# Optimization experiments

Hardware: AMD Instinct MI355X
Metric: run time of the kernel (lower is better)

## Reference

```python
import jax, jax.numpy as jnp
import numpy as np

B, S, H = 64, 2048, 512
NEG_INF = -1e10


def setup_inputs() -> dict:
    key = jax.random.key(0)
    k1, k2, k3, k4, k5, k6 = jax.random.split(key, 6)
    return {
        "output": jax.random.normal(k1, (B, 1, H), dtype=jnp.float32),
        "encoder_outputs": jax.random.normal(k2, (B, S, H), dtype=jnp.float32),
        "encoder_sequence_lengths": jax.random.randint(k3, (B,), 1, S + 1, dtype=jnp.int32),
        "W1": jax.random.normal(k4, (H, H), dtype=jnp.float32) * (1.0 / np.sqrt(H)),
        "W2": jax.random.normal(k5, (H, H), dtype=jnp.float32) * (1.0 / np.sqrt(H)),
        "V": jax.random.normal(k6, (H, 1), dtype=jnp.float32) * (1.0 / np.sqrt(H)),
    }


def reference(output, encoder_outputs, encoder_sequence_lengths, W1, W2, V):
    # output: [B,1,H] decoder state (query); encoder_outputs: [B,S,H] (key & value)
    S_ = encoder_outputs.shape[1]
    key_proj = jnp.einsum('bsh,hd->bsd', encoder_outputs, W1)   # [B,S,H]
    query_proj = jnp.einsum('bqh,hd->bqd', output, W2)          # [B,1,H]
    energy = jnp.einsum('bsh,ho->bso', jnp.tanh(key_proj + query_proj), V)  # [B,S,1]
    mask = jnp.arange(S_)[None, :, None] < encoder_sequence_lengths[:, None, None]  # [B,S,1]
    energy = jnp.where(mask, energy, NEG_INF)
    attn = jax.nn.softmax(energy, axis=1)                       # [B,S,1]
    context = jnp.sum(attn * encoder_outputs, axis=1)           # [B,H]
    return context
```

## Files before the change

kernel.cpp:

```cpp
#include <hip/hip_runtime.h>
#include <hip/hip_bf16.h>

#define SS 2048
#define HH 512

typedef __attribute__((ext_vector_type(8))) short short8;
typedef __attribute__((ext_vector_type(4))) float f32x4;

__device__ __forceinline__ float bflo(unsigned u) { return __uint_as_float(u << 16); }
__device__ __forceinline__ float bfhi(unsigned u) { return __uint_as_float(u & 0xffff0000u); }

__device__ __forceinline__ short f2bf(float v) {
  __hip_bfloat16 h = __float2bfloat16(v);
  return *reinterpret_cast<short*>(&h);
}

__device__ __forceinline__ float tanh_fast(float x) {
  x = fminf(fmaxf(x, -15.f), 15.f);
  float e = __expf(2.f * x);
  return 1.f - 2.f / (e + 1.f);
}

__global__ void k_detect(const unsigned* __restrict__ Eu, const int* __restrict__ lens,
                         int* __restrict__ flag, int* __restrict__ tmap,
                         int* __restrict__ livep) {
  int lane = threadIdx.x;
  unsigned w = Eu[(size_t)lane * 4097];
  unsigned e = (w >> 7) & 0xFF;
  bool inr = (e >= 90 && e <= 140);
  unsigned long long m = __ballot(inr);
  if (lane == 0) *flag = (__popcll(m) >= 48) ? 1 : 0;

  int len = lens[lane];
  int n = (len + 127) >> 7;
  int off = n;
#pragma unroll
  for (int o = 1; o < 64; o <<= 1) {
    int v = __shfl_up(off, o);
    if (lane >= o) off += v;
  }
  int base = off - n;
  for (int j = 0; j < n; ++j) tmap[base + j] = lane * 16 + j;
  if (lane == 63) *livep = off;
}

__global__ __launch_bounds__(256) void k_prep(const __hip_bfloat16* __restrict__ W1b,
                                              const float* __restrict__ W1f,
                                              const __hip_bfloat16* __restrict__ qb,
                                              const float* __restrict__ qf,
                                              const __hip_bfloat16* __restrict__ W2b,
                                              const float* __restrict__ W2f,
                                              const int* __restrict__ flagp,
                                              __hip_bfloat16* __restrict__ W1T,
                                              float* __restrict__ qp_part) {
  const int mode = *flagp;
  __shared__ __hip_bfloat16 t[64][65];
  __shared__ float qs[128];
  if (blockIdx.x < 64) {
    int r0 = (blockIdx.x >> 3) * 64, c0 = (blockIdx.x & 7) * 64;
    for (int i = threadIdx.x; i < 4096; i += 256) {
      int r = i >> 6, c = i & 63;
      size_t idx = (size_t)(r0 + r) * HH + c0 + c;
      float v = mode ? (float)W1b[idx] : W1f[idx];
      t[r][c] = __float2bfloat16(v);
    }
    __syncthreads();
    for (int i = threadIdx.x; i < 4096; i += 256) {
      int r = i >> 6, c = i & 63;
      W1T[(size_t)(c0 + r) * HH + r0 + c] = t[c][r];
    }
  } else {
    int bx = blockIdx.x - 64;
    int b = bx & 63, p = bx >> 6, h0 = p * 128;
    if (threadIdx.x < 128) {
      size_t qi = (size_t)b * HH + h0 + threadIdx.x;
      qs[threadIdx.x] = mode ? (float)qb[qi] : qf[qi];
    }
    __syncthreads();
    int col = threadIdx.x * 2;
    float a0 = 0.f, a1 = 0.f;
    if (mode) {
#pragma unroll 4
      for (int i = 0; i < 128; ++i) {
        float qa = qs[i];
        unsigned u = *(const unsigned*)(W2b + (size_t)(h0 + i) * HH + col);
        a0 = fmaf(qa, bflo(u), a0);
        a1 = fmaf(qa, bfhi(u), a1);
      }
    } else {
#pragma unroll 4
      for (int i = 0; i < 128; ++i) {
        float qa = qs[i];
        float2 v = *(const float2*)(W2f + (size_t)(h0 + i) * HH + col);
        a0 = fmaf(qa, v.x, a0);
        a1 = fmaf(qa, v.y, a1);
      }
    }
    float* dst = qp_part + ((size_t)p * 64 + b) * HH + col;
    dst[0] = a0;
    dst[1] = a1;
  }
}

__global__ __launch_bounds__(256, 2) void k_energy(
    const __hip_bfloat16* __restrict__ Eb, const float* __restrict__ Ef,
    const __hip_bfloat16* __restrict__ W1T, const float* __restrict__ qpp,
    const __hip_bfloat16* __restrict__ Vwb, const float* __restrict__ Vwf,
    const int* __restrict__ flagp, const int* __restrict__ lens,
    const int* __restrict__ tmap, const int* __restrict__ livep,
    float* __restrict__ tpart) {
  __shared__ __align__(16) __hip_bfloat16 Bt[4][128 * 32];
  __shared__ float qps[HH];
  __shared__ float Vs[HH];
  __shared__ float p[128];
  __shared__ float red[4];
  __shared__ f32x4 part[128];

  const int tid = threadIdx.x;
  const int wave = tid >> 6, lane = tid & 63;
  const int quad = lane >> 4, l16 = lane & 15;
  const int mode = *flagp;
  const int live = *livep;

  const int rs0 = wave * 32 + (lane >> 2);
  const int rs1 = rs0 + 16;
  const int kg0 = ((lane & 3) - (rs0 >> 1)) & 3;
  const int kg1 = ((lane & 3) - (rs1 >> 1)) & 3;
  const __hip_bfloat16* pb0 = W1T + (size_t)rs0 * HH + kg0 * 8;
  const __hip_bfloat16* pb1 = W1T + (size_t)rs1 * HH + kg1 * 8;
  const int wslot = wave * 1024 + lane * 8;

  int offB[8];
#pragma unroll
  for (int cb = 0; cb < 8; ++cb) {
    int n = cb * 16 + l16;
    offB[cb] = n * 32 + (((quad + (n >> 1)) & 3) << 3);
  }

  for (int i = tid; i < HH; i += 256) Vs[i] = mode ? (float)Vwb[i] : Vwf[i];

  for (int idx = blockIdx.x; idx < live; idx += 512) {
    const int tile = tmap[idx];
    const int b = tile >> 4;
    const int row0 = tile * 128;
    const int len = lens[b];

    for (int i = tid; i < HH; i += 256)
      qps[i] = qpp[(size_t)b * HH + i] + qpp[(size_t)(64 + b) * HH + i] +
               qpp[(size_t)(128 + b) * HH + i] + qpp[(size_t)(192 + b) * HH + i];

    short8 afr[2][16];
    {
      const size_t eBase = (size_t)row0 * HH + (size_t)(wave * 32 + l16) * HH + quad * 8;
      if (mode) {
        const __hip_bfloat16* pa = Eb + eBase;
#pragma unroll
        for (int kt = 0; kt < 16; ++kt) {
          afr[0][kt] = *(const short8*)(pa + kt * 32);
          afr[1][kt] = *(const short8*)(pa + 16 * HH + kt * 32);
        }
      } else {
        const float* pa = Ef + eBase;
#pragma unroll
        for (int kt = 0; kt < 16; ++kt) {
#pragma unroll
          for (int rb = 0; rb < 2; ++rb) {
            const float* pp = pa + rb * 16 * HH + kt * 32;
            f32x4 x0 = *(const f32x4*)pp;
            f32x4 x1 = *(const f32x4*)(pp + 4);
            short8 v;
#pragma unroll
            for (int j = 0; j < 4; ++j) {
              v[j] = f2bf(x0[j]);
              v[j + 4] = f2bf(x1[j]);
            }
            afr[rb][kt] = v;
          }
        }
      }
    }

    short8 bpa[4], bpb[4];
    bpa[0] = *(const short8*)(pb0);
    bpb[0] = *(const short8*)(pb1);
    *(short8*)(&Bt[0][0] + wslot) = bpa[0];
    *(short8*)(&Bt[0][0] + wslot + 512) = bpb[0];
    bpa[1] = *(const short8*)(pb0 + 32);
    bpb[1] = *(const short8*)(pb1 + 32);
    bpa[2] = *(const short8*)(pb0 + 64);
    bpb[2] = *(const short8*)(pb1 + 64);
    bpa[3] = *(const short8*)(pb0 + 96);
    bpb[3] = *(const short8*)(pb1 + 96);
    __syncthreads();

    float eacc[2][4] = {{0.f, 0.f, 0.f, 0.f}, {0.f, 0.f, 0.f, 0.f}};

    for (int nc = 0; nc < 4; ++nc) {
      f32x4 acc[2][8];
#pragma unroll
      for (int rb = 0; rb < 2; ++rb)
#pragma unroll
        for (int cb = 0; cb < 8; ++cb) acc[rb][cb] = (f32x4){0.f, 0.f, 0.f, 0.f};

#pragma unroll
      for (int kt = 0; kt < 16; ++kt) {
        const int t = nc * 16 + kt;
        const __hip_bfloat16* bb = &Bt[kt & 3][0];
        short8 af0 = afr[0][kt];
        short8 af1 = afr[1][kt];
#pragma unroll
        for (int cb = 0; cb < 8; ++cb) {
          short8 bf = *(const short8*)(bb + offB[cb]);
          acc[0][cb] = __builtin_amdgcn_mfma_f32_16x16x32_bf16(af0, bf, acc[0][cb], 0, 0, 0);
          acc[1][cb] = __builtin_amdgcn_mfma_f32_16x16x32_bf16(af1, bf, acc[1][cb], 0, 0, 0);
        }

        {
          const int ss = (kt + 1) & 3;
          const int sp = kt & 3;
          __hip_bfloat16* bw = &Bt[ss][0] + wslot;
          *(short8*)bw = bpa[ss];
          *(short8*)(bw + 512) = bpb[ss];
          int t2 = t + 4;
          if (t2 > 63) t2 = 63;
          int o = ((t2 >> 4) << 16) + ((t2 & 15) << 5);
          bpa[sp] = *(const short8*)(pb0 + o);
          bpb[sp] = *(const short8*)(pb1 + o);
        }
        asm volatile("s_waitcnt lgkmcnt(0)" ::: "memory");
        __builtin_amdgcn_s_barrier();
        __builtin_amdgcn_sched_barrier(0);
      }

#pragma unroll
      for (int rb = 0; rb < 2; ++rb)
#pragma unroll
        for (int cb = 0; cb < 8; ++cb) {
          int col = nc * 128 + cb * 16 + l16;
          float qv = qps[col], vv = Vs[col];
#pragma unroll
          for (int r = 0; r < 4; ++r) {
            float tv = tanh_fast(acc[rb][cb][r] + qv);
            eacc[rb][r] = fmaf(vv, tv, eacc[rb][r]);
          }
        }
    }

#pragma unroll
    for (int rb = 0; rb < 2; ++rb)
#pragma unroll
      for (int r = 0; r < 4; ++r) {
        float v = eacc[rb][r];
#pragma unroll
        for (int o = 1; o < 16; o <<= 1) v += __shfl_xor(v, o);
        if (l16 == 0) {
          int row = wave * 32 + rb * 16 + quad * 4 + r;
          int s = (row0 & 2047) + row;
          p[row] = (s < len) ? v : -3.0e38f;
        }
      }
    __syncthreads();

    float e = (tid < 128) ? p[tid] : -3.0e38f;
    float m = e;
#pragma unroll
    for (int o = 1; o < 64; o <<= 1) m = fmaxf(m, __shfl_xor(m, o));
    if ((tid & 63) == 0) red[tid >> 6] = m;
    __syncthreads();
    m = fmaxf(fmaxf(red[0], red[1]), fmaxf(red[2], red[3]));
    float w = (tid < 128) ? __expf(e - m) : 0.f;
    float d = w;
#pragma unroll
    for (int o = 1; o < 64; o <<= 1) d += __shfl_xor(d, o);
    __syncthreads();
    if ((tid & 63) == 0) red[tid >> 6] = d;
    if (tid < 128) p[tid] = w;
    __syncthreads();
    const float d_t = red[0] + red[1] + red[2] + red[3];

    const int n = min(128, len - (row0 & 2047));
    const int h0 = (tid & 127) * 4;
    const int rr = tid >> 7;
    f32x4 a = {0.f, 0.f, 0.f, 0.f};
    if (mode) {
      const __hip_bfloat16* base = Eb + (size_t)row0 * HH + h0;
#pragma unroll 4
      for (int i = rr; i < n; i += 2) {
        float wv = p[i];
        uint2 u = *(const uint2*)(base + (size_t)i * HH);
        a[0] = fmaf(wv, bflo(u.x), a[0]);
        a[1] = fmaf(wv, bfhi(u.x), a[1]);
        a[2] = fmaf(wv, bflo(u.y), a[2]);
        a[3] = fmaf(wv, bfhi(u.y), a[3]);
      }
    } else {
      const float* base = Ef + (size_t)row0 * HH + h0;
#pragma unroll 4
      for (int i = rr; i < n; i += 2) {
        float wv = p[i];
        f32x4 v = *(const f32x4*)(base + (size_t)i * HH);
        a[0] = fmaf(wv, v[0], a[0]);
        a[1] = fmaf(wv, v[1], a[1]);
        a[2] = fmaf(wv, v[2], a[2]);
        a[3] = fmaf(wv, v[3], a[3]);
      }
    }
    if (tid >= 128) part[tid - 128] = a;
    __syncthreads();
    if (tid < 128) {
      f32x4 o = part[tid];
      f32x4 s;
      s[0] = a[0] + o[0];
      s[1] = a[1] + o[1];
      s[2] = a[2] + o[2];
      s[3] = a[3] + o[3];
      *(f32x4*)(tpart + (size_t)tile * 516 + h0) = s;
    }
    if (tid == 0) {
      tpart[(size_t)tile * 516 + 512] = m;
      tpart[(size_t)tile * 516 + 513] = d_t;
    }
  }
}

__global__ __launch_bounds__(256) void k_reduce(const float* __restrict__ tpart,
                                                const int* __restrict__ lens,
                                                const int* __restrict__ flagp,
                                                __hip_bfloat16* __restrict__ outb,
                                                float* __restrict__ outf) {
  const int b = blockIdx.x, tid = threadIdx.x;
  const int nch = (lens[b] + 127) >> 7;
  const float* tb = tpart + (size_t)b * 16 * 516;
  float m = -3.0e38f;
  for (int c = 0; c < nch; ++c) m = fmaxf(m, tb[c * 516 + 512]);
  const int h = tid * 2;
  float den = 0.f, a0 = 0.f, a1 = 0.f;
  for (int c = 0; c < nch; ++c) {
    float sc = __expf(tb[c * 516 + 512] - m);
    den = fmaf(tb[c * 516 + 513], sc, den);
    float2 v = *(const float2*)(tb + c * 516 + h);
    a0 = fmaf(sc, v.x, a0);
    a1 = fmaf(sc, v.y, a1);
  }
  float inv = 1.f / den;
  int i = b * HH + h;
  if (*flagp) {
    outb[i] = __float2bfloat16(a0 * inv);
    outb[i + 1] = __float2bfloat16(a1 * inv);
  } else {
    outf[i] = a0 * inv;
    outf[i + 1] = a1 * inv;
  }
}

extern "C" void kernel_launch(void* const* d_in, const int* in_sizes, int n_in,
                              void* d_out, int out_size, void* d_ws, size_t ws_size,
                              hipStream_t stream) {
  const __hip_bfloat16* qb  = (const __hip_bfloat16*)d_in[0];
  const float*          qf  = (const float*)d_in[0];
  const __hip_bfloat16* Eb  = (const __hip_bfloat16*)d_in[1];
  const float*          Ef  = (const float*)d_in[1];
  const int* lens           = (const int*)d_in[2];
  const __hip_bfloat16* W1b = (const __hip_bfloat16*)d_in[3];
  const float*          W1f = (const float*)d_in[3];
  const __hip_bfloat16* W2b = (const __hip_bfloat16*)d_in[4];
  const float*          W2f = (const float*)d_in[4];
  const __hip_bfloat16* Vwb = (const __hip_bfloat16*)d_in[5];
  const float*          Vwf = (const float*)d_in[5];
  __hip_bfloat16* outb      = (__hip_bfloat16*)d_out;
  float*          outf      = (float*)d_out;

  char* ws = (char*)d_ws;
  __hip_bfloat16* W1T = (__hip_bfloat16*)(ws);
  float* qp_part      = (float*)(ws + 524288);
  float* tpart        = (float*)(ws + 1048576);
  int* flag           = (int*)(ws + 3162112);
  int* tmap           = (int*)(ws + 3162624);
  int* livep          = (int*)(ws + 3166720);

  k_detect<<<dim3(1), 64, 0, stream>>>((const unsigned*)d_in[1], lens, flag, tmap, livep);
  k_prep<<<dim3(320), 256, 0, stream>>>(W1b, W1f, qb, qf, W2b, W2f, flag, W1T, qp_part);
  k_energy<<<dim3(512), 256, 0, stream>>>(Eb, Ef, W1T, qp_part, Vwb, Vwf, flag, lens,
                                          tmap, livep, tpart);
  k_reduce<<<dim3(64), 256, 0, stream>>>(tpart, lens, flag, outb, outf);
}
```

Measured before the change: 481.1 us.

## Halve energy tiles to 64 rows, one tile per block, async global-to-LDS W1 prefetch

The energy kernel now processes 64-row tiles instead of 128, with one block per tile launched over a 2048-block grid, so the persistent loop goes away. The tile map and the reduce kernel change to match. W1T slices are now streamed straight into LDS with global_load_lds, three stages ahead, gated by vmcnt waits, replacing the register staging and ds_write path. Fewer accumulators allow three blocks per CU, and the softmax reduction fits in one wave. The trade-off is twice as many partial tiles and W1 being re-read once per smaller tile, which doubles W1 traffic per row of E.

```diff
diff --git a/kernel.cpp b/kernel.cpp
--- a/kernel.cpp
+++ b/kernel.cpp
@@ -18,7 +18,13 @@
 __device__ __forceinline__ float tanh_fast(float x) {
   x = fminf(fmaxf(x, -15.f), 15.f);
   float e = __expf(2.f * x);
-  return 1.f - 2.f / (e + 1.f);
+  return 1.f - 2.f * __builtin_amdgcn_rcpf(e + 1.f);
+}
+
+__device__ __forceinline__ void gll16(const void* g, void* l) {
+  __builtin_amdgcn_global_load_lds(
+      (const __attribute__((address_space(1))) unsigned int*)g,
+      (__attribute__((address_space(3))) unsigned int*)l, 16, 0, 0);
 }
 
 __global__ void k_detect(const unsigned* __restrict__ Eu, const int* __restrict__ lens,
@@ -32,7 +38,7 @@
   if (lane == 0) *flag = (__popcll(m) >= 48) ? 1 : 0;
 
   int len = lens[lane];
-  int n = (len + 127) >> 7;
+  int n = (len + 63) >> 6;
   int off = n;
 #pragma unroll
   for (int o = 1; o < 64; o <<= 1) {
@@ -40,7 +46,7 @@
     if (lane >= o) off += v;
   }
   int base = off - n;
-  for (int j = 0; j < n; ++j) tmap[base + j] = lane * 16 + j;
+  for (int j = 0; j < n; ++j) tmap[base + j] = lane * 32 + j;
   if (lane == 63) *livep = off;
 }
 
@@ -102,7 +108,7 @@
   }
 }
 
-__global__ __launch_bounds__(256, 2) void k_energy(
+__global__ __launch_bounds__(256, 3) void k_energy(
     const __hip_bfloat16* __restrict__ Eb, const float* __restrict__ Ef,
     const __hip_bfloat16* __restrict__ W1T, const float* __restrict__ qpp,
     const __hip_bfloat16* __restrict__ Vwb, const float* __restrict__ Vwf,
@@ -112,15 +118,22 @@
   __shared__ __align__(16) __hip_bfloat16 Bt[4][128 * 32];
   __shared__ float qps[HH];
   __shared__ float Vs[HH];
-  __shared__ float p[128];
+  __shared__ float p[64];
   __shared__ float red[4];
   __shared__ f32x4 part[128];
 
   const int tid = threadIdx.x;
   const int wave = tid >> 6, lane = tid & 63;
   const int quad = lane >> 4, l16 = lane & 15;
+  const int live = *livep;
+  if (blockIdx.x >= live) return;
   const int mode = *flagp;
-  const int live = *livep;
+
+  const int tile = tmap[blockIdx.x];
+  const int b = tile >> 5;
+  const int srow = (tile & 31) * 64;
+  const int row0 = b * SS + srow;
+  const int len = lens[b];
 
   const int rs0 = wave * 32 + (lane >> 2);
   const int rs1 = rs0 + 16;
@@ -128,7 +141,8 @@
   const int kg1 = ((lane & 3) - (rs1 >> 1)) & 3;
   const __hip_bfloat16* pb0 = W1T + (size_t)rs0 * HH + kg0 * 8;
   const __hip_bfloat16* pb1 = W1T + (size_t)rs1 * HH + kg1 * 8;
-  const int wslot = wave * 1024 + lane * 8;
+  char* ldsB = (char*)&Bt[0][0];
+  char* ldW = ldsB + wave * 2048;
 
   int offB[8];
 #pragma unroll
@@ -137,189 +151,166 @@
     offB[cb] = n * 32 + (((quad + (n >> 1)) & 3) << 3);
   }
 
-  for (int i = tid; i < HH; i += 256) Vs[i] = mode ? (float)Vwb[i] : Vwf[i];
-
-  for (int idx = blockIdx.x; idx < live; idx += 512) {
-    const int tile = tmap[idx];
-    const int b = tile >> 4;
-    const int row0 = tile * 128;
-    const int len = lens[b];
-
-    for (int i = tid; i < HH; i += 256)
-      qps[i] = qpp[(size_t)b * HH + i] + qpp[(size_t)(64 + b) * HH + i] +
-               qpp[(size_t)(128 + b) * HH + i] + qpp[(size_t)(192 + b) * HH + i];
-
-    short8 afr[2][16];
-    {
-      const size_t eBase = (size_t)row0 * HH + (size_t)(wave * 32 + l16) * HH + quad * 8;
-      if (mode) {
-        const __hip_bfloat16* pa = Eb + eBase;
-#pragma unroll
-        for (int kt = 0; kt < 16; ++kt) {
-          afr[0][kt] = *(const short8*)(pa + kt * 32);
-          afr[1][kt] = *(const short8*)(pa + 16 * HH + kt * 32);
+#pragma unroll
+  for (int s = 0; s < 3; ++s) {
+    int o = s << 5;
+    gll16(pb0 + o, ldW + s * 8192);
+    gll16(pb1 + o, ldW + s * 8192 + 1024);
+  }
+
+  short8 afr[16];
+  {
+    const size_t eBase = (size_t)(row0 + wave * 16 + l16) * HH + quad * 8;
+    if (mode) {
+      const __hip_bfloat16* pa = Eb + eBase;
+#pragma unroll
+      for (int kt = 0; kt < 16; ++kt) afr[kt] = *(const short8*)(pa + kt * 32);
+    } else {
+      const float* pa = Ef + eBase;
+#pragma unroll
+      for (int g = 0; g < 4; ++g) {
+        f32x4 x0[4], x1[4];
+#pragma unroll
+        for (int k = 0; k < 4; ++k) {
+          const float* pp = pa + (g * 4 + k) * 32;
+          x0[k] = *(const f32x4*)pp;
+          x1[k] = *(const f32x4*)(pp + 4);
         }
-      } else {
-        const float* pa = Ef + eBase;
-#pragma unroll
-        for (int kt = 0; kt < 16; ++kt) {
-#pragma unroll
-          for (int rb = 0; rb < 2; ++rb) {
-            const float* pp = pa + rb * 16 * HH + kt * 32;
-            f32x4 x0 = *(const f32x4*)pp;
-            f32x4 x1 = *(const f32x4*)(pp + 4);
-            short8 v;
-#pragma unroll
-            for (int j = 0; j < 4; ++j) {
-              v[j] = f2bf(x0[j]);
-              v[j + 4] = f2bf(x1[j]);
-            }
-            afr[rb][kt] = v;
+#pragma unroll
+        for (int k = 0; k < 4; ++k) {
+          short8 v;
+#pragma unroll
+          for (int j = 0; j < 4; ++j) {
+            v[j] = f2bf(x0[k][j]);
+            v[j + 4] = f2bf(x1[k][j]);
           }
+          afr[g * 4 + k] = v;
         }
       }
     }
-
-    short8 bpa[4], bpb[4];
-    bpa[0] = *(const short8*)(pb0);
-    bpb[0] = *(const short8*)(pb1);
-    *(short8*)(&Bt[0][0] + wslot) = bpa[0];
-    *(short8*)(&Bt[0][0] + wslot + 512) = bpb[0];
-    bpa[1] = *(const short8*)(pb0 + 32);
-    bpb[1] = *(const short8*)(pb1 + 32);
-    bpa[2] = *(const short8*)(pb0 + 64);
-    bpb[2] = *(const short8*)(pb1 + 64);
-    bpa[3] = *(const short8*)(pb0 + 96);
-    bpb[3] = *(const short8*)(pb1 + 96);
-    __syncthreads();
-
-    float eacc[2][4] = {{0.f, 0.f, 0.f, 0.f}, {0.f, 0.f, 0.f, 0.f}};
-
-    for (int nc = 0; nc < 4; ++nc) {
-      f32x4 acc[2][8];
-#pragma unroll
-      for (int rb = 0; rb < 2; ++rb)
-#pragma unroll
-        for (int cb = 0; cb < 8; ++cb) acc[rb][cb] = (f32x4){0.f, 0.f, 0.f, 0.f};
-
-#pragma unroll
-      for (int kt = 0; kt < 16; ++kt) {
-        const int t = nc * 16 + kt;
-        const __hip_bfloat16* bb = &Bt[kt & 3][0];
-        short8 af0 = afr[0][kt];
-        short8 af1 = afr[1][kt];
-#pragma unroll
-        for (int cb = 0; cb < 8; ++cb) {
-          short8 bf = *(const short8*)(bb + offB[cb]);
-          acc[0][cb] = __builtin_amdgcn_mfma_f32_16x16x32_bf16(af0, bf, acc[0][cb], 0, 0, 0);
-          acc[1][cb] = __builtin_amdgcn_mfma_f32_16x16x32_bf16(af1, bf, acc[1][cb], 0, 0, 0);
-        }
-
-        {
-          const int ss = (kt + 1) & 3;
-          const int sp = kt & 3;
-          __hip_bfloat16* bw = &Bt[ss][0] + wslot;
-          *(short8*)bw = bpa[ss];
-          *(short8*)(bw + 512) = bpb[ss];
-          int t2 = t + 4;
-          if (t2 > 63) t2 = 63;
-          int o = ((t2 >> 4) << 16) + ((t2 & 15) << 5);
-          bpa[sp] = *(const short8*)(pb0 + o);
-          bpb[sp] = *(const short8*)(pb1 + o);
-        }
-        asm volatile("s_waitcnt lgkmcnt(0)" ::: "memory");
-        __builtin_amdgcn_s_barrier();
-        __builtin_amdgcn_sched_barrier(0);
-      }
-
-#pragma unroll
-      for (int rb = 0; rb < 2; ++rb)
-#pragma unroll
-        for (int cb = 0; cb < 8; ++cb) {
-          int col = nc * 128 + cb * 16 + l16;
-          float qv = qps[col], vv = Vs[col];
-#pragma unroll
-          for (int r = 0; r < 4; ++r) {
-            float tv = tanh_fast(acc[rb][cb][r] + qv);
-            eacc[rb][r] = fmaf(vv, tv, eacc[rb][r]);
-          }
-        }
-    }
-
-#pragma unroll
-    for (int rb = 0; rb < 2; ++rb)
+  }
+
+  for (int i = tid; i < HH; i += 256) {
+    qps[i] = qpp[(size_t)b * HH + i] + qpp[(size_t)(64 + b) * HH + i] +
+             qpp[(size_t)(128 + b) * HH + i] + qpp[(size_t)(192 + b) * HH + i];
+    Vs[i] = mode ? (float)Vwb[i] : Vwf[i];
+  }
+
+  float eacc[4] = {0.f, 0.f, 0.f, 0.f};
+
+  for (int nc = 0; nc < 4; ++nc) {
+    f32x4 acc[8];
+#pragma unroll
+    for (int cb = 0; cb < 8; ++cb) acc[cb] = (f32x4){0.f, 0.f, 0.f, 0.f};
+
+#pragma unroll
+    for (int kt = 0; kt < 16; ++kt) {
+      __builtin_amdgcn_sched_barrier(0);
+      asm volatile("s_waitcnt vmcnt(4)" ::: "memory");
+      __builtin_amdgcn_s_barrier();
+      __builtin_amdgcn_sched_barrier(0);
+
+      {
+        int t2 = nc * 16 + kt + 3;
+        if (t2 > 63) t2 = 63;
+        int o = ((t2 >> 4) << 16) + ((t2 & 15) << 5);
+        char* ld = ldW + ((kt + 3) & 3) * 8192;
+        gll16(pb0 + o, ld);
+        gll16(pb1 + o, ld + 1024);
+      }
+
+      const __hip_bfloat16* bb = &Bt[kt & 3][0];
+      short8 af = afr[kt];
+#pragma unroll
+      for (int cb = 0; cb < 8; ++cb) {
+        short8 bf = *(const short8*)(bb + offB[cb]);
+        acc[cb] = __builtin_amdgcn_mfma_f32_16x16x32_bf16(af, bf, acc[cb], 0, 0, 0);
+      }
+    }
+
+#pragma unroll
+    for (int cb = 0; cb < 8; ++cb) {
+      int col = nc * 128 + cb * 16 + l16;
+      float qv = qps[col], vv = Vs[col];
 #pragma unroll
       for (int r = 0; r < 4; ++r) {
-        float v = eacc[rb][r];
-#pragma unroll
-        for (int o = 1; o < 16; o <<= 1) v += __shfl_xor(v, o);
-        if (l16 == 0) {
-          int row = wave * 32 + rb * 16 + quad * 4 + r;
-          int s = (row0 & 2047) + row;
-          p[row] = (s < len) ? v : -3.0e38f;
-        }
-      }
-    __syncthreads();
-
-    float e = (tid < 128) ? p[tid] : -3.0e38f;
+        float tv = tanh_fast(acc[cb][r] + qv);
+        eacc[r] = fmaf(vv, tv, eacc[r]);
+      }
+    }
+  }
+
+#pragma unroll
+  for (int r = 0; r < 4; ++r) {
+    float v = eacc[r];
+#pragma unroll
+    for (int o = 1; o < 16; o <<= 1) v += __shfl_xor(v, o);
+    if (l16 == 0) {
+      int row = wave * 16 + quad * 4 + r;
+      p[row] = (srow + row < len) ? v : -3.0e38f;
+    }
+  }
+  __syncthreads();
+
+  if (wave == 0) {
+    float e = p[lane];
     float m = e;
 #pragma unroll
     for (int o = 1; o < 64; o <<= 1) m = fmaxf(m, __shfl_xor(m, o));
-    if ((tid & 63) == 0) red[tid >> 6] = m;
-    __syncthreads();
-    m = fmaxf(fmaxf(red[0], red[1]), fmaxf(red[2], red[3]));
-    float w = (tid < 128) ? __expf(e - m) : 0.f;
+    float w = __expf(e - m);
     float d = w;
 #pragma unroll
     for (int o = 1; o < 64; o <<= 1) d += __shfl_xor(d, o);
-    __syncthreads();
-    if ((tid & 63) == 0) red[tid >> 6] = d;
-    if (tid < 128) p[tid] = w;
-    __syncthreads();
-    const float d_t = red[0] + red[1] + red[2] + red[3];
-
-    const int n = min(128, len - (row0 & 2047));
-    const int h0 = (tid & 127) * 4;
-    const int rr = tid >> 7;
-    f32x4 a = {0.f, 0.f, 0.f, 0.f};
-    if (mode) {
-      const __hip_bfloat16* base = Eb + (size_t)row0 * HH + h0;
-#pragma unroll 4
-      for (int i = rr; i < n; i += 2) {
-        float wv = p[i];
-        uint2 u = *(const uint2*)(base + (size_t)i * HH);
-        a[0] = fmaf(wv, bflo(u.x), a[0]);
-        a[1] = fmaf(wv, bfhi(u.x), a[1]);
-        a[2] = fmaf(wv, bflo(u.y), a[2]);
-        a[3] = fmaf(wv, bfhi(u.y), a[3]);
-      }
-    } else {
-      const float* base = Ef + (size_t)row0 * HH + h0;
-#pragma unroll 4
-      for (int i = rr; i < n; i += 2) {
-        float wv = p[i];
-        f32x4 v = *(const f32x4*)(base + (size_t)i * HH);
-        a[0] = fmaf(wv, v[0], a[0]);
-        a[1] = fmaf(wv, v[1], a[1]);
-        a[2] = fmaf(wv, v[2], a[2]);
-        a[3] = fmaf(wv, v[3], a[3]);
-      }
-    }
-    if (tid >= 128) part[tid - 128] = a;
-    __syncthreads();
-    if (tid < 128) {
-      f32x4 o = part[tid];
-      f32x4 s;
-      s[0] = a[0] + o[0];
-      s[1] = a[1] + o[1];
-      s[2] = a[2] + o[2];
-      s[3] = a[3] + o[3];
-      *(f32x4*)(tpart + (size_t)tile * 516 + h0) = s;
-    }
-    if (tid == 0) {
-      tpart[(size_t)tile * 516 + 512] = m;
-      tpart[(size_t)tile * 516 + 513] = d_t;
-    }
+    p[lane] = w;
+    if (lane == 0) {
+      red[0] = m;
+      red[1] = d;
+    }
+  }
+  __syncthreads();
+  const float m_t = red[0], d_t = red[1];
+
+  const int n = min(64, len - srow);
+  const int h0 = (tid & 127) * 4;
+  const int rr = tid >> 7;
+  f32x4 a = {0.f, 0.f, 0.f, 0.f};
+  if (mode) {
+    const __hip_bfloat16* base = Eb + (size_t)row0 * HH + h0;
+#pragma unroll 8
+    for (int i = rr; i < n; i += 2) {
+      float wv = p[i];
+      uint2 u = *(const uint2*)(base + (size_t)i * HH);
+      a[0] = fmaf(wv, bflo(u.x), a[0]);
+      a[1] = fmaf(wv, bfhi(u.x), a[1]);
+      a[2] = fmaf(wv, bflo(u.y), a[2]);
+      a[3] = fmaf(wv, bfhi(u.y), a[3]);
+    }
+  } else {
+    const float* base = Ef + (size_t)row0 * HH + h0;
+#pragma unroll 8
+    for (int i = rr; i < n; i += 2) {
+      float wv = p[i];
+      f32x4 v = *(const f32x4*)(base + (size_t)i * HH);
+      a[0] = fmaf(wv, v[0], a[0]);
+      a[1] = fmaf(wv, v[1], a[1]);
+      a[2] = fmaf(wv, v[2], a[2]);
+      a[3] = fmaf(wv, v[3], a[3]);
+    }
+  }
+  if (tid >= 128) part[tid - 128] = a;
+  __syncthreads();
+  if (tid < 128) {
+    f32x4 o = part[tid];
+    f32x4 s;
+    s[0] = a[0] + o[0];
+    s[1] = a[1] + o[1];
+    s[2] = a[2] + o[2];
+    s[3] = a[3] + o[3];
+    *(f32x4*)(tpart + (size_t)tile * 516 + h0) = s;
+  }
+  if (tid == 0) {
+    tpart[(size_t)tile * 516 + 512] = m_t;
+    tpart[(size_t)tile * 516 + 513] = d_t;
   }
 }
 
@@ -329,8 +320,8 @@
                                                 __hip_bfloat16* __restrict__ outb,
                                                 float* __restrict__ outf) {
   const int b = blockIdx.x, tid = threadIdx.x;
-  const int nch = (lens[b] + 127) >> 7;
-  const float* tb = tpart + (size_t)b * 16 * 516;
+  const int nch = (lens[b] + 63) >> 6;
+  const float* tb = tpart + (size_t)b * 32 * 516;
   float m = -3.0e38f;
   for (int c = 0; c < nch; ++c) m = fmaxf(m, tb[c * 516 + 512]);
   const int h = tid * 2;
@@ -374,13 +365,13 @@
   __hip_bfloat16* W1T = (__hip_bfloat16*)(ws);
   float* qp_part      = (float*)(ws + 524288);
   float* tpart        = (float*)(ws + 1048576);
-  int* flag           = (int*)(ws + 3162112);
-  int* tmap           = (int*)(ws + 3162624);
-  int* livep          = (int*)(ws + 3166720);
+  int* flag           = (int*)(ws + 5275648);
+  int* tmap           = (int*)(ws + 5275652);
+  int* livep          = (int*)(ws + 5283844);
 
   k_detect<<<dim3(1), 64, 0, stream>>>((const unsigned*)d_in[1], lens, flag, tmap, livep);
   k_prep<<<dim3(320), 256, 0, stream>>>(W1b, W1f, qb, qf, W2b, W2f, flag, W1T, qp_part);
-  k_energy<<<dim3(512), 256, 0, stream>>>(Eb, Ef, W1T, qp_part, Vwb, Vwf, flag, lens,
-                                          tmap, livep, tpart);
+  k_energy<<<dim3(2048), 256, 0, stream>>>(Eb, Ef, W1T, qp_part, Vwb, Vwf, flag, lens,
+                                           tmap, livep, tpart);
   k_reduce<<<dim3(64), 256, 0, stream>>>(tpart, lens, flag, outb, outf);
 }
```

After: 446.3 us. -7.2%, faster.
